# Kernel tuning notes

Hardware: AMD Instinct MI355X
Metric: run time of the kernel (lower is better)

## Reference

```python
import jax, jax.numpy as jnp
import numpy as np

DIM = 1024
HEADS = 16
SCALE = DIM ** -0.5  # NOTE: original uses full dim, not head dim


def setup_inputs() -> dict:
    key = jax.random.key(0)
    k1, k2, k3, k4 = jax.random.split(key, 4)
    x = jax.random.normal(k1, (2, 2048, DIM), dtype=jnp.float32)
    # torch nn.Linear(dim, 3*dim, bias=False): y = x @ W_qkv (stored here as [dim, 3*dim])
    w_qkv = jax.random.normal(k2, (DIM, 3 * DIM), dtype=jnp.float32) * (DIM ** -0.5)
    w_out = jax.random.normal(k3, (DIM, DIM), dtype=jnp.float32) * (DIM ** -0.5)
    b_out = jax.random.normal(k4, (DIM,), dtype=jnp.float32) * 0.01
    return {"x": x, "w_qkv": w_qkv, "w_out": w_out, "b_out": b_out}


def reference(x, w_qkv, w_out, b_out):
    b, n, d = x.shape
    h = HEADS
    hd = d // h
    qkv = x @ w_qkv  # [b, n, 3*d]
    # last dim layout is (qkv, h, hd) per rearrange 'b n (qkv h d) -> qkv b h n d'
    qkv = qkv.reshape(b, n, 3, h, hd)
    q, k, v = (jnp.moveaxis(qkv, (2, 3), (0, 2))[i] for i in range(3))  # each [b, h, n, hd]
    dots = jnp.einsum('bhid,bhjd->bhij', q, k) * SCALE
    causal_mask = jnp.triu(jnp.ones((n, n), dtype=bool), k=1)
    dots = jnp.where(causal_mask, -jnp.inf, dots)
    attn = jax.nn.softmax(dots, axis=-1)
    out = jnp.einsum('bhij,bhjd->bhid', attn, v)
    out = jnp.moveaxis(out, 1, 2).reshape(b, n, d)  # 'b h n d -> b n (h d)'
    return out @ w_out + b_out
```

## Files before the change

### kernel.cpp

```cpp
#include <hip/hip_runtime.h>

typedef __attribute__((ext_vector_type(8))) short bf16x8;
typedef __attribute__((ext_vector_type(4))) float f32x4;
typedef unsigned short u16;
typedef unsigned int u32;

#define SEQ 2048
#define NHEAD 16
#define EXP2_SCALE 0.045084219f

__device__ __forceinline__ u16 f2bf(float f){
  u32 u = __builtin_bit_cast(u32, f);
  u += 0x7FFFu + ((u >> 16) & 1u);
  return (u16)(u >> 16);
}

__device__ __forceinline__ void gl16(const u16* g, u16* l){
  __builtin_amdgcn_global_load_lds(
      (__attribute__((address_space(1))) void*)(unsigned long long)(const void*)g,
      (__attribute__((address_space(3))) void*)(unsigned)(unsigned long long)(const void*)l,
      16, 0, 0);
}

__global__ __launch_bounds__(256) void prep(const float* __restrict__ x,
                                            const float* __restrict__ w_qkv,
                                            const float* __restrict__ w_out,
                                            u16* __restrict__ xb,
                                            u16* __restrict__ wqkvT,
                                            u16* __restrict__ woutT){
  __shared__ u16 t[32][33];
  const int bid = blockIdx.x;
  if (bid < 4096){
    int i = (bid * 256 + threadIdx.x) << 2;
    float4 v = *(const float4*)&x[i];
    ushort4 o;
    o.x = f2bf(v.x); o.y = f2bf(v.y); o.z = f2bf(v.z); o.w = f2bf(v.w);
    *(ushort4*)&xb[i] = o;
    return;
  }
  const float* src; u16* dst; int R, C, bx, by;
  if (bid < 7168){ int tt = bid - 4096; src = w_qkv; dst = wqkvT; R = 1024; C = 3072; bx = tt % 96; by = tt / 96; }
  else           { int tt = bid - 7168; src = w_out; dst = woutT; R = 1024; C = 1024; bx = tt % 32; by = tt / 32; }
  const int c0 = bx << 5, r0 = by << 5;
  const int tx = threadIdx.x & 31, tg = threadIdx.x >> 5;
  #pragma unroll
  for (int i = 0; i < 4; i++){
    int r = (tg << 2) + i;
    t[r][tx] = f2bf(src[(size_t)(r0 + r) * C + (c0 + tx)]);
  }
  __syncthreads();
  #pragma unroll
  for (int i = 0; i < 4; i++){
    int c = (tg << 2) + i;
    dst[(size_t)(c0 + c) * R + (r0 + tx)] = t[tx][c];
  }
}

__global__ __launch_bounds__(256) void gemm_qkv(const u16* __restrict__ A,
                                                const u16* __restrict__ Bt,
                                                u16* __restrict__ Qo,
                                                u16* __restrict__ Ko,
                                                u16* __restrict__ Vto){
  __shared__ u16 As[128 * 64];
  __shared__ u16 Bs[128 * 64];
  const int tid = threadIdx.x;
  const int lane = tid & 63, wid = tid >> 6;
  const int l15 = lane & 15, quad = lane >> 4;
  const int wm = wid >> 1, wn = wid & 1;
  const int bm = blockIdx.y << 7, bn = blockIdx.x << 7;
  const int qkv_idx = bn >> 10;

  const int lr = lane >> 3;
  const int cc = (lane & 7) ^ lr;
  const u16* gA0 = A  + (size_t)(bm + wid * 32 + lr) * 1024 + (cc << 3);
  const u16* gB0 = Bt + (size_t)(bn + wid * 32 + lr) * 1024 + (cc << 3);
  u16* lA0 = &As[wid * 2048];
  u16* lB0 = &Bs[wid * 2048];

  f32x4 acc[4][4];
  #pragma unroll
  for (int i = 0; i < 4; i++)
    #pragma unroll
    for (int j = 0; j < 4; j++) acc[i][j] = (f32x4){0.f, 0.f, 0.f, 0.f};

  for (int k0 = 0; k0 < 1024; k0 += 64){
    #pragma unroll
    for (int t = 0; t < 4; t++){
      gl16(gA0 + k0 + t * 8192, lA0 + t * 512);
      gl16(gB0 + k0 + t * 8192, lB0 + t * 512);
    }
    __syncthreads();
    #pragma unroll
    for (int hf = 0; hf < 2; hf++){
      bf16x8 af[4], bfr[4];
      #pragma unroll
      for (int mt = 0; mt < 4; mt++){
        int row = wm * 64 + mt * 16 + l15;
        af[mt] = *(const bf16x8*)&As[row * 64 + (((hf * 4 + quad) ^ (row & 7)) << 3)];
      }
      #pragma unroll
      for (int nt = 0; nt < 4; nt++){
        int row = wn * 64 + nt * 16 + l15;
        bfr[nt] = *(const bf16x8*)&Bs[row * 64 + (((hf * 4 + quad) ^ (row & 7)) << 3)];
      }
      #pragma unroll
      for (int mt = 0; mt < 4; mt++)
        #pragma unroll
        for (int nt = 0; nt < 4; nt++)
          acc[mt][nt] = __builtin_amdgcn_mfma_f32_16x16x32_bf16(bfr[nt], af[mt], acc[mt][nt], 0, 0, 0);
    }
    __syncthreads();
  }

  if (qkv_idx != 2){
    const float qs = (qkv_idx == 0) ? EXP2_SCALE : 1.0f;
    u16* dst = (qkv_idx == 0) ? Qo : Ko;
    #pragma unroll
    for (int mt = 0; mt < 4; mt++){
      int xr = bm + wm * 64 + mt * 16 + l15;
      int b = xr >> 11, pos = xr & 2047;
      #pragma unroll
      for (int nt = 0; nt < 4; nt++){
        int c0 = bn + wn * 64 + nt * 16 + quad * 4;
        int head = (c0 & 1023) >> 6, hd0 = c0 & 63;
        size_t bhh = ((size_t)(b * NHEAD + head)) << 17;
        ushort4 w;
        w.x = f2bf(acc[mt][nt][0] * qs); w.y = f2bf(acc[mt][nt][1] * qs);
        w.z = f2bf(acc[mt][nt][2] * qs); w.w = f2bf(acc[mt][nt][3] * qs);
        *(ushort4*)&dst[bhh + ((size_t)pos << 6) + hd0] = w;
      }
    }
  } else {
    #pragma unroll
    for (int mt = 0; mt < 4; mt++){
      int xr = bm + wm * 64 + mt * 16 + l15;
      int b = xr >> 11, pos = xr & 2047;
      #pragma unroll
      for (int nt = 0; nt < 4; nt++){
        #pragma unroll
        for (int r = 0; r < 4; r++){
          int c = bn + wn * 64 + nt * 16 + quad * 4 + r;
          int head = (c & 1023) >> 6, hd_i = c & 63;
          size_t bhh = ((size_t)(b * NHEAD + head)) << 17;
          Vto[bhh + ((size_t)hd_i << 11) + pos] = f2bf(acc[mt][nt][r]);
        }
      }
    }
  }
}

__global__ __launch_bounds__(512, 4) void attn_kernel(const u16* __restrict__ Q,
                                                      const u16* __restrict__ K,
                                                      const u16* __restrict__ Vt,
                                                      u16* __restrict__ Oo){
  __shared__ u16 Ks[128 * 64];
  __shared__ u16 Vts[64 * 128];
  __shared__ u16 Ps[8][16 * 136];
  const int tid = threadIdx.x;
  const int lane = tid & 63, wid = tid >> 6;
  const int l15 = lane & 15, quad = lane >> 4;
  const int bh = blockIdx.x & 31;
  const int j = blockIdx.x >> 5;
  const int qt2 = (j < 8) ? (15 - j) : (j - 8);
  const size_t base = ((size_t)bh) << 17;
  const int b = bh >> 4, h = bh & 15;

  const u16* qsrc = Q + base + ((size_t)((qt2 << 7) + wid * 16 + l15) << 6) + quad * 8;
  const bf16x8 bq0 = *(const bf16x8*)qsrc;
  const bf16x8 bq1 = *(const bf16x8*)(qsrc + 32);

  const int rK = wid * 16 + (lane >> 3);
  const int cK = (lane & 7) ^ (rK & 7);
  const u16* gK0 = K + base + ((size_t)rK << 6) + (cK << 3);
  u16* lK = &Ks[wid * 1024];
  const u16* gV[2];
  #pragma unroll
  for (int t = 0; t < 2; t++){
    int rv = wid * 8 + t * 4 + (lane >> 4);
    int cv = (lane & 15) ^ (rv & 15);
    gV[t] = Vt + base + (size_t)rv * 2048 + (cv << 3);
  }
  u16* lV = &Vts[wid * 1024];

  f32x4 o[4];
  #pragma unroll
  for (int dt = 0; dt < 4; dt++) o[dt] = (f32x4){0.f, 0.f, 0.f, 0.f};
  float lsum = 0.f;
  const int qpos = (qt2 << 7) + wid * 16 + l15;
  const int jt_max = qt2;
  u16* Pw = &Ps[wid][0];

  auto kv_iter = [&](const int jt, const bool diag) __attribute__((always_inline)) {
    const u16* gk = gK0 + (size_t)jt * 8192;
    gl16(gk,       lK);
    gl16(gk + 512, lK + 512);
    gl16(gV[0] + (jt << 7), lV);
    gl16(gV[1] + (jt << 7), lV + 512);
    __syncthreads();

    f32x4 st[8];
    #pragma unroll
    for (int mt = 0; mt < 8; mt++) st[mt] = (f32x4){0.f, 0.f, 0.f, 0.f};
    #pragma unroll
    for (int mt = 0; mt < 8; mt++){
      int kvr = mt * 16 + l15;
      bf16x8 ak0 = *(const bf16x8*)&Ks[kvr * 64 + ((quad ^ (kvr & 7)) << 3)];
      st[mt] = __builtin_amdgcn_mfma_f32_16x16x32_bf16(ak0, bq0, st[mt], 0, 0, 0);
      bf16x8 ak1 = *(const bf16x8*)&Ks[kvr * 64 + (((4 + quad) ^ (kvr & 7)) << 3)];
      st[mt] = __builtin_amdgcn_mfma_f32_16x16x32_bf16(ak1, bq1, st[mt], 0, 0, 0);
    }

    #pragma unroll
    for (int mt = 0; mt < 8; mt++){
      float pr[4];
      #pragma unroll
      for (int r = 0; r < 4; r++){
        float w = st[mt][r];
        if (diag){
          int kv = (jt << 7) + mt * 16 + quad * 4 + r;
          if (kv > qpos) w = -INFINITY;
        }
        pr[r] = __builtin_amdgcn_exp2f(w);
      }
      lsum += (pr[0] + pr[1]) + (pr[2] + pr[3]);
      u32 a0 = __builtin_bit_cast(u32, pr[0]) + 0x8000u;
      u32 a1 = __builtin_bit_cast(u32, pr[1]) + 0x8000u;
      u32 a2 = __builtin_bit_cast(u32, pr[2]) + 0x8000u;
      u32 a3 = __builtin_bit_cast(u32, pr[3]) + 0x8000u;
      uint2 pk;
      pk.x = __builtin_amdgcn_perm(a1, a0, 0x07060302u);
      pk.y = __builtin_amdgcn_perm(a3, a2, 0x07060302u);
      *(uint2*)&Pw[l15 * 136 + mt * 16 + quad * 4] = pk;
    }

    #pragma unroll
    for (int ks = 0; ks < 4; ks++){
      bf16x8 bp = *(const bf16x8*)&Pw[l15 * 136 + ks * 32 + quad * 8];
      #pragma unroll
      for (int dt = 0; dt < 4; dt++){
        int dr = dt * 16 + l15;
        bf16x8 av = *(const bf16x8*)&Vts[dr * 128 + (((ks * 4 + quad) ^ (dr & 15)) << 3)];
        o[dt] = __builtin_amdgcn_mfma_f32_16x16x32_bf16(av, bp, o[dt], 0, 0, 0);
      }
    }
    __syncthreads();
  };

  for (int jt = 0; jt < jt_max; jt++) kv_iter(jt, false);
  kv_iter(jt_max, true);

  lsum += __shfl_xor(lsum, 16);
  lsum += __shfl_xor(lsum, 32);
  float inv = 1.f / lsum;
  const size_t orow = (size_t)((b << 11) + qpos) * 1024 + h * 64;
  #pragma unroll
  for (int dt = 0; dt < 4; dt++){
    ushort4 w;
    w.x = f2bf(o[dt][0] * inv); w.y = f2bf(o[dt][1] * inv);
    w.z = f2bf(o[dt][2] * inv); w.w = f2bf(o[dt][3] * inv);
    *(ushort4*)&Oo[orow + dt * 16 + quad * 4] = w;
  }
}

__global__ __launch_bounds__(256) void gemm_out(const u16* __restrict__ A,
                                                const u16* __restrict__ Bt,
                                                const float* __restrict__ bias,
                                                float* __restrict__ out){
  __shared__ u16 As[128 * 64];
  __shared__ u16 Bs[128 * 64];
  const int tid = threadIdx.x;
  const int lane = tid & 63, wid = tid >> 6;
  const int l15 = lane & 15, quad = lane >> 4;
  const int wm = wid >> 1, wn = wid & 1;
  const int bm = blockIdx.y << 7, bn = blockIdx.x << 7;

  const int lr = lane >> 3;
  const int cc = (lane & 7) ^ lr;
  const u16* gA0 = A  + (size_t)(bm + wid * 32 + lr) * 1024 + (cc << 3);
  const u16* gB0 = Bt + (size_t)(bn + wid * 32 + lr) * 1024 + (cc << 3);
  u16* lA0 = &As[wid * 2048];
  u16* lB0 = &Bs[wid * 2048];

  f32x4 acc[4][4];
  #pragma unroll
  for (int i = 0; i < 4; i++)
    #pragma unroll
    for (int j = 0; j < 4; j++) acc[i][j] = (f32x4){0.f, 0.f, 0.f, 0.f};

  for (int k0 = 0; k0 < 1024; k0 += 64){
    #pragma unroll
    for (int t = 0; t < 4; t++){
      gl16(gA0 + k0 + t * 8192, lA0 + t * 512);
      gl16(gB0 + k0 + t * 8192, lB0 + t * 512);
    }
    __syncthreads();
    #pragma unroll
    for (int hf = 0; hf < 2; hf++){
      bf16x8 af[4], bfr[4];
      #pragma unroll
      for (int mt = 0; mt < 4; mt++){
        int row = wm * 64 + mt * 16 + l15;
        af[mt] = *(const bf16x8*)&As[row * 64 + (((hf * 4 + quad) ^ (row & 7)) << 3)];
      }
      #pragma unroll
      for (int nt = 0; nt < 4; nt++){
        int row = wn * 64 + nt * 16 + l15;
        bfr[nt] = *(const bf16x8*)&Bs[row * 64 + (((hf * 4 + quad) ^ (row & 7)) << 3)];
      }
      #pragma unroll
      for (int mt = 0; mt < 4; mt++)
        #pragma unroll
        for (int nt = 0; nt < 4; nt++)
          acc[mt][nt] = __builtin_amdgcn_mfma_f32_16x16x32_bf16(bfr[nt], af[mt], acc[mt][nt], 0, 0, 0);
    }
    __syncthreads();
  }

  #pragma unroll
  for (int nt = 0; nt < 4; nt++){
    int c0 = bn + wn * 64 + nt * 16 + quad * 4;
    float4 bv = *(const float4*)&bias[c0];
    #pragma unroll
    for (int mt = 0; mt < 4; mt++){
      int row = bm + wm * 64 + mt * 16 + l15;
      float4 w;
      w.x = acc[mt][nt][0] + bv.x; w.y = acc[mt][nt][1] + bv.y;
      w.z = acc[mt][nt][2] + bv.z; w.w = acc[mt][nt][3] + bv.w;
      *(float4*)&out[(size_t)row * 1024 + c0] = w;
    }
  }
}

extern "C" void kernel_launch(void* const* d_in, const int* in_sizes, int n_in,
                              void* d_out, int out_size, void* d_ws, size_t ws_size,
                              hipStream_t stream){
  const float* x     = (const float*)d_in[0];
  const float* w_qkv = (const float*)d_in[1];
  const float* w_out = (const float*)d_in[2];
  const float* b_out = (const float*)d_in[3];
  float* out = (float*)d_out;

  char* ws = (char*)d_ws;
  u16* xb    = (u16*)(ws);
  u16* wqkvT = (u16*)(ws + (8u  << 20));
  u16* woutT = (u16*)(ws + (14u << 20));
  u16* Qb    = (u16*)(ws + (16u << 20));
  u16* Kb    = (u16*)(ws + (24u << 20));
  u16* Vtb   = (u16*)(ws + (32u << 20));
  u16* attn  = (u16*)(ws + (40u << 20));

  prep<<<8192, 256, 0, stream>>>(x, w_qkv, w_out, xb, wqkvT, woutT);
  gemm_qkv<<<dim3(24, 32), 256, 0, stream>>>(xb, wqkvT, Qb, Kb, Vtb);
  attn_kernel<<<dim3(512), 512, 0, stream>>>(Qb, Kb, Vtb, attn);
  gemm_out<<<dim3(8, 32), 256, 0, stream>>>(attn, woutT, b_out, out);
}
```

Before: 177.9 us.

## Remap GEMM blocks per XCD and split attention into 64-row query tiles

Both GEMMs now use a 1D grid whose block index is remapped so that consecutive blocks on the same XCD share M-rows, aiming at better L2 reuse of the A and B tiles. The attention kernel drops from 512 threads with 128 query rows per block to 256 threads with 64 rows per block. Grid size doubles to 1024 blocks, ordered largest-first by causal work, which replaces the previous paired balancing. Each wave now loads twice as much K and V into LDS per tile. Smaller blocks give finer load balance and higher occupancy, but the same K/V tiles are fetched by twice as many blocks.

Measured after the change: 176.6 us. Within noise of the previous version (-0.8%).

```diff
diff --git a/kernel.cpp b/kernel.cpp
--- a/kernel.cpp
+++ b/kernel.cpp
@@ -67,7 +67,10 @@
   const int lane = tid & 63, wid = tid >> 6;
   const int l15 = lane & 15, quad = lane >> 4;
   const int wm = wid >> 1, wn = wid & 1;
-  const int bm = blockIdx.y << 7, bn = blockIdx.x << 7;
+  const int bid = blockIdx.x;
+  const int xcd = bid & 7, t8 = bid >> 3;
+  const int bm = ((xcd << 2) + (t8 & 3)) << 7;
+  const int bn = (t8 >> 2) << 7;
   const int qkv_idx = bn >> 10;
 
   const int lr = lane >> 3;
@@ -149,53 +152,52 @@
   }
 }
 
-__global__ __launch_bounds__(512, 4) void attn_kernel(const u16* __restrict__ Q,
-                                                      const u16* __restrict__ K,
-                                                      const u16* __restrict__ Vt,
-                                                      u16* __restrict__ Oo){
+__global__ __launch_bounds__(256) void attn_kernel(const u16* __restrict__ Q,
+                                                   const u16* __restrict__ K,
+                                                   const u16* __restrict__ Vt,
+                                                   u16* __restrict__ Oo){
   __shared__ u16 Ks[128 * 64];
   __shared__ u16 Vts[64 * 128];
-  __shared__ u16 Ps[8][16 * 136];
+  __shared__ u16 Ps[4][16 * 136];
   const int tid = threadIdx.x;
   const int lane = tid & 63, wid = tid >> 6;
   const int l15 = lane & 15, quad = lane >> 4;
   const int bh = blockIdx.x & 31;
-  const int j = blockIdx.x >> 5;
-  const int qt2 = (j < 8) ? (15 - j) : (j - 8);
+  const int qt = 31 - (blockIdx.x >> 5);
   const size_t base = ((size_t)bh) << 17;
   const int b = bh >> 4, h = bh & 15;
 
-  const u16* qsrc = Q + base + ((size_t)((qt2 << 7) + wid * 16 + l15) << 6) + quad * 8;
+  const u16* qsrc = Q + base + ((size_t)((qt << 6) + wid * 16 + l15) << 6) + quad * 8;
   const bf16x8 bq0 = *(const bf16x8*)qsrc;
   const bf16x8 bq1 = *(const bf16x8*)(qsrc + 32);
 
-  const int rK = wid * 16 + (lane >> 3);
+  const int rK = wid * 32 + (lane >> 3);
   const int cK = (lane & 7) ^ (rK & 7);
   const u16* gK0 = K + base + ((size_t)rK << 6) + (cK << 3);
-  u16* lK = &Ks[wid * 1024];
-  const u16* gV[2];
-  #pragma unroll
-  for (int t = 0; t < 2; t++){
-    int rv = wid * 8 + t * 4 + (lane >> 4);
+  u16* lK = &Ks[wid * 2048];
+  const u16* gV[4];
+  #pragma unroll
+  for (int t = 0; t < 4; t++){
+    int rv = wid * 16 + t * 4 + (lane >> 4);
     int cv = (lane & 15) ^ (rv & 15);
     gV[t] = Vt + base + (size_t)rv * 2048 + (cv << 3);
   }
-  u16* lV = &Vts[wid * 1024];
+  u16* lV = &Vts[wid * 2048];
 
   f32x4 o[4];
   #pragma unroll
   for (int dt = 0; dt < 4; dt++) o[dt] = (f32x4){0.f, 0.f, 0.f, 0.f};
   float lsum = 0.f;
-  const int qpos = (qt2 << 7) + wid * 16 + l15;
-  const int jt_max = qt2;
+  const int qpos = (qt << 6) + wid * 16 + l15;
+  const int jt_max = qt >> 1;
   u16* Pw = &Ps[wid][0];
 
   auto kv_iter = [&](const int jt, const bool diag) __attribute__((always_inline)) {
     const u16* gk = gK0 + (size_t)jt * 8192;
-    gl16(gk,       lK);
-    gl16(gk + 512, lK + 512);
-    gl16(gV[0] + (jt << 7), lV);
-    gl16(gV[1] + (jt << 7), lV + 512);
+    #pragma unroll
+    for (int t = 0; t < 4; t++) gl16(gk + t * 512, lK + t * 512);
+    #pragma unroll
+    for (int t = 0; t < 4; t++) gl16(gV[t] + (jt << 7), lV + t * 512);
     __syncthreads();
 
     f32x4 st[8];
@@ -272,7 +274,10 @@
   const int lane = tid & 63, wid = tid >> 6;
   const int l15 = lane & 15, quad = lane >> 4;
   const int wm = wid >> 1, wn = wid & 1;
-  const int bm = blockIdx.y << 7, bn = blockIdx.x << 7;
+  const int bid = blockIdx.x;
+  const int xcd = bid & 7, t8 = bid >> 3;
+  const int bm = ((xcd << 2) + (t8 & 3)) << 7;
+  const int bn = (t8 >> 2) << 7;
 
   const int lr = lane >> 3;
   const int cc = (lane & 7) ^ lr;
@@ -350,7 +355,7 @@
   u16* attn  = (u16*)(ws + (40u << 20));
 
   prep<<<8192, 256, 0, stream>>>(x, w_qkv, w_out, xb, wqkvT, woutT);
-  gemm_qkv<<<dim3(24, 32), 256, 0, stream>>>(xb, wqkvT, Qb, Kb, Vtb);
-  attn_kernel<<<dim3(512), 512, 0, stream>>>(Qb, Kb, Vtb, attn);
-  gemm_out<<<dim3(8, 32), 256, 0, stream>>>(attn, woutT, b_out, out);
-}
+  gemm_qkv<<<768, 256, 0, stream>>>(xb, wqkvT, Qb, Kb, Vtb);
+  attn_kernel<<<dim3(1024), 256, 0, stream>>>(Qb, Kb, Vtb, attn);
+  gemm_out<<<256, 256, 0, stream>>>(attn, woutT, b_out, out);
+}
```
